# Kernel optimization log

Hardware: AMD Instinct MI355X
Metric: run time of the kernel (lower is better)

The kernel has to match this reference:

```python
import jax, jax.numpy as jnp
import numpy as np

B, L, DL, DM, K = 8192, 1, 1024, 1024, 8


def setup_inputs() -> dict:
    key = jax.random.key(0)
    ks = jax.random.split(key, 8)
    s = lambda k, shape, sc=1.0: jax.random.normal(k, shape, jnp.float32) * sc
    return {
        "l_hidden": s(ks[0], (B, L, DL)),
        "m_hidden": s(ks[1], (B, L, DM)),
        "G_l_m": s(ks[2], (DL, K, DM)),   # randn'd each fwd in torch; exposed as input
        "G_m_l": s(ks[3], (DM, K, DL)),
        "l_fc1_w": s(ks[4], (256, DL), 0.02),
        "l_fc1_b": jnp.zeros((256,), jnp.float32),
        "l_fc2_w": s(ks[5], (DL, 256), 0.02),
        "l_fc2_b": jnp.zeros((DL,), jnp.float32),
        "m_fc1_w": s(ks[6], (128, DM), 0.02),
        "m_fc1_b": jnp.zeros((128,), jnp.float32),
        "m_fc2_w": s(ks[7], (DM, 128), 0.02),
        "m_fc2_b": jnp.zeros((DM,), jnp.float32),
    }


def _cross(h_a, h_b, G, g_vec):
    """One direction of the cross-share unit.
    h_a: [B,L,Da], h_b: [B,L,Db], G: [Da,K,Db], g_vec: [B,L,Da]. L must be 1.
    Broadcasts G over batch instead of torch's .repeat (same math, no 256GB copy).
    """
    b, l, da = h_a.shape
    k = G.shape[1]
    # l_hidden @ reshape(G, [Da, K*Db]) -> reshape to [B, L*K, Db]
    s = jnp.einsum('bld,dke->blke', h_a, G).reshape(b, l * k, -1)      # [B,L*K,Db]
    # tanh( shared @ h_b^T ) -> [B, L*K, L]
    t = jnp.tanh(jnp.einsum('bke,bse->bks', s, h_b))                    # [B,L*K,L]
    # reshape [B,L,K,L] -> permute [B,L,L,K] -> [B,L*L,K]
    t = t.reshape(b, l, k, l).transpose(0, 1, 3, 2).reshape(b, l * l, k)
    g = jnp.tile(g_vec, (1, k, 1))                                      # [B,L*K,Da] (L=1 -> [B,K,Da])
    vec = jnp.matmul(t, g)                                              # [B,L*L,Da]
    attn = jax.nn.softmax(vec, axis=-1)
    out = h_a + attn * h_a
    return out, attn


def reference(l_hidden, m_hidden, G_l_m, G_m_l,
              l_fc1_w, l_fc1_b, l_fc2_w, l_fc2_b,
              m_fc1_w, m_fc1_b, m_fc2_w, m_fc2_b):
    # dropout(0.3) is identity in eval mode
    G_vec_l = (l_hidden @ l_fc1_w.T + l_fc1_b) @ l_fc2_w.T + l_fc2_b   # [B,L,DL]
    G_vec_m = (m_hidden @ m_fc1_w.T + m_fc1_b) @ m_fc2_w.T + m_fc2_b   # [B,L,DM]
    l_out, l_attn = _cross(l_hidden, m_hidden, G_l_m, G_vec_l)
    m_out, m_attn = _cross(m_hidden, l_hidden, G_m_l, G_vec_m)
    return l_out, m_out, l_attn, m_attn
```

## Files before the change

kernel.cpp:

```cpp
#include <hip/hip_runtime.h>


#define NB 8192
#define DD 1024

typedef __bf16 bf16x8 __attribute__((ext_vector_type(8)));
typedef float f32x4 __attribute__((ext_vector_type(4)));

__device__ __forceinline__ unsigned short f2bf(float f) {
  unsigned u = __float_as_uint(f);
  u += 0x7FFFu + ((u >> 16) & 1u);
  return (unsigned short)(u >> 16);
}
__device__ __forceinline__ float bf2f(unsigned short h) {
  return __uint_as_float(((unsigned)h) << 16);
}

__global__ __launch_bounds__(256) void split_cast_k(
    const float* __restrict__ in, unsigned short* __restrict__ hi,
    unsigned short* __restrict__ lo, int n4) {
  int i = blockIdx.x * 256 + threadIdx.x;
  if (i >= n4) return;
  float4 v = reinterpret_cast<const float4*>(in)[i];
  float vv[4] = {v.x, v.y, v.z, v.w};
  unsigned short hh[4], ll[4];
#pragma unroll
  for (int c = 0; c < 4; ++c) {
    hh[c] = f2bf(vv[c]);
    ll[c] = f2bf(vv[c] - bf2f(hh[c]));
  }
  reinterpret_cast<ushort4*>(hi)[i] = make_ushort4(hh[0], hh[1], hh[2], hh[3]);
  reinterpret_cast<ushort4*>(lo)[i] = make_ushort4(ll[0], ll[1], ll[2], ll[3]);
}

__global__ __launch_bounds__(256) void transpose_split_k(
    const float* __restrict__ G, unsigned short* __restrict__ bhi,
    unsigned short* __restrict__ blo) {
  __shared__ float t[32][33];
  int c0 = blockIdx.x * 32;
  int d0 = blockIdx.y * 32;
  int tx = threadIdx.x & 31;
  int tg = threadIdx.x >> 5;
#pragma unroll
  for (int s = 0; s < 4; ++s) {
    int dr = tg * 4 + s;
    t[dr][tx] = G[(size_t)(d0 + dr) * 8192 + c0 + tx];
  }
  __syncthreads();
#pragma unroll
  for (int s = 0; s < 4; ++s) {
    int cr = tg * 4 + s;
    float v = t[tx][cr];
    size_t o = (size_t)(c0 + cr) * 1024 + d0 + tx;
    unsigned short h = f2bf(v);
    bhi[o] = h;
    blo[o] = f2bf(v - bf2f(h));
  }
}

__global__ __launch_bounds__(256) void wct_k(
    const float* __restrict__ w1, const float* __restrict__ b1,
    const float* __restrict__ w2, const float* __restrict__ b2, int J,
    unsigned short* __restrict__ bhi, unsigned short* __restrict__ blo,
    float* __restrict__ bc) {
  __shared__ float w2row[256];
  int n = blockIdx.x;
  int tid = threadIdx.x;
  if (tid < J) w2row[tid] = w2[n * J + tid];
  __syncthreads();
#pragma unroll
  for (int s = 0; s < 4; ++s) {
    int i = tid + s * 256;
    float acc = 0.f;
    for (int j = 0; j < J; ++j) acc = fmaf(w2row[j], w1[j * 1024 + i], acc);
    size_t o = (size_t)(8192 + n) * 1024 + i;
    unsigned short h = f2bf(acc);
    bhi[o] = h;
    blo[o] = f2bf(acc - bf2f(h));
  }
  if (tid == 0) {
    float acc = 0.f;
    for (int j = 0; j < J; ++j) acc = fmaf(w2row[j], b1[j], acc);
    bc[n] = acc + b2[n];
  }
}

#define SBAR() do { asm volatile("" ::: "memory"); __builtin_amdgcn_s_barrier(); asm volatile("" ::: "memory"); } while (0)
#define WAITV4() asm volatile("s_waitcnt vmcnt(4)" ::: "memory")
#define WAITV6() asm volatile("s_waitcnt vmcnt(6)" ::: "memory")

#define GLOAD(SRC, DST)                                              \
  __builtin_amdgcn_global_load_lds(                                  \
      (const __attribute__((address_space(1))) void*)(SRC),          \
      (__attribute__((address_space(3))) void*)(lds + (DST)), 16, 0, 0)

__global__ __launch_bounds__(512, 2) void gemm_k(
    const unsigned short* __restrict__ Ahi_, const unsigned short* __restrict__ Alo_,
    const unsigned short* __restrict__ Bhi_, const unsigned short* __restrict__ Blo_,
    const float* __restrict__ hb, float* __restrict__ gvec, float* __restrict__ x) {
  __shared__ __align__(16) char lds[147456];
  const char* Ah = (const char*)Ahi_;
  const char* Al = (const char*)Alo_;
  const char* Bh = (const char*)Bhi_;
  const char* Bl = (const char*)Blo_;

  const int tid = threadIdx.x;
  const int lane = tid & 63;
  const int wid = tid >> 6;
  const int wm = wid >> 2, wn = wid & 3;

  const int bid = blockIdx.x;
  const int xcd = bid & 7, j = bid >> 3;
  const int by = xcd * 4 + (j & 3);
  const int bx = j >> 2;
  const int m0 = by * 256, n0 = bx * 256;
  const int nt = (n0 >= 8192) ? 16 : 48;

  const int rowl = tid >> 3;
  const int colsw = ((tid & 7) ^ ((tid >> 3) & 7)) << 4;
  const int s0 = ((lane >> 4) ^ (lane & 7)) << 4;
  const int s1 = s0 ^ 64;

  f32x4 acc[4][4][2] = {};

  auto stage = [&](int tile, int q) {
    if (tile < nt) {
      const int seg = tile >> 4;
      const char* mat;
      int rowbase, dst;
      if (q < 2) {
        mat = (seg == 1) ? Al : Ah;
        rowbase = m0 + q * 128;
        dst = (tile & 1) * 32768 + q * 16384;
      } else {
        mat = (seg == 2) ? Bl : Bh;
        rowbase = n0 + (q - 2) * 128;
        dst = 65536 + (tile & 1) * 32768 + (q - 2) * 16384;
      }
      const char* src = mat + (size_t)(rowbase + rowl) * 2048 + ((tile & 15) << 7) + colsw;
      dst += wid * 1024;
      GLOAD(src, dst);
      GLOAD(src + 64 * 2048, dst + 8192);
    } else {
      const char* src = Ah + (size_t)(m0 + rowl) * 2048 + colsw;
      const int d2 = 131072 + wid * 1024;
      GLOAD(src, d2);
      GLOAD(src + 64 * 2048, d2 + 8192);
    }
  };

  auto ldA = [&](bf16x8 (*d)[2], int qa, int cb) {
    const char* p = lds + cb + qa * 16384 + (wm * 64 + (lane & 15)) * 128;
#pragma unroll
    for (int f = 0; f < 4; ++f) {
      d[f][0] = *reinterpret_cast<const bf16x8*>(p + f * 2048 + s0);
      d[f][1] = *reinterpret_cast<const bf16x8*>(p + f * 2048 + s1);
    }
  };
  auto ldB = [&](bf16x8 (*d)[2], int qb, int cb) {
    const char* p = lds + 65536 + cb + qb * 16384 + (wn * 32 + (lane & 15)) * 128;
#pragma unroll
    for (int g = 0; g < 2; ++g) {
      d[g][0] = *reinterpret_cast<const bf16x8*>(p + g * 2048 + s0);
      d[g][1] = *reinterpret_cast<const bf16x8*>(p + g * 2048 + s1);
    }
  };
  auto mm = [&](f32x4 (*ac)[2], bf16x8 (*aa)[2], bf16x8 (*bb)[2]) {
#pragma unroll
    for (int f = 0; f < 4; ++f)
#pragma unroll
      for (int g = 0; g < 2; ++g) {
        ac[f][g] = __builtin_amdgcn_mfma_f32_16x16x32_bf16(aa[f][0], bb[g][0], ac[f][g], 0, 0, 0);
        ac[f][g] = __builtin_amdgcn_mfma_f32_16x16x32_bf16(aa[f][1], bb[g][1], ac[f][g], 0, 0, 0);
      }
  };

  stage(0, 0); stage(0, 2);
  stage(0, 3);
  stage(0, 1);
  WAITV4();
  SBAR();

  bf16x8 af[4][2], af2[4][2], bv[2][2], bv2[2][2];
  for (int t = 0; t < nt; ++t) {
    const int cb = (t & 1) * 32768;
    ldA(af, 0, cb);
    ldB(bv, 0, cb);
    stage(t + 1, 0); stage(t + 1, 2);
    SBAR();
    __builtin_amdgcn_s_setprio(1);
    mm(acc[0], af, bv);
    __builtin_amdgcn_s_setprio(0);
    WAITV6();
    SBAR();
    ldB(bv2, 1, cb);
    stage(t + 1, 3);
    SBAR();
    __builtin_amdgcn_s_setprio(1);
    mm(acc[1], af, bv2);
    __builtin_amdgcn_s_setprio(0);
    WAITV6();
    SBAR();
    ldA(af2, 1, cb);
    stage(t + 1, 1);
    SBAR();
    __builtin_amdgcn_s_setprio(1);
    mm(acc[2], af2, bv2);
    __builtin_amdgcn_s_setprio(0);
    SBAR();
    ldB(bv, 0, cb);
    SBAR();
    __builtin_amdgcn_s_setprio(1);
    mm(acc[3], af2, bv);
    __builtin_amdgcn_s_setprio(0);
    WAITV4();
    SBAR();
  }

  const int coll = lane & 15;
  const int rg = (lane >> 4) * 4;
  if (n0 >= 8192) {
#pragma unroll
    for (int q = 0; q < 4; ++q) {
      const int qm = (q >= 2);
      const int qn = (q == 1 || q == 2);
#pragma unroll
      for (int f = 0; f < 4; ++f)
#pragma unroll
        for (int r = 0; r < 4; ++r) {
          const int row = m0 + qm * 128 + wm * 64 + f * 16 + rg + r;
#pragma unroll
          for (int g = 0; g < 2; ++g) {
            const int gcol = (n0 - 8192) + qn * 128 + wn * 32 + g * 16 + coll;
            gvec[(size_t)row * 1024 + gcol] = acc[q][f][g][r];
          }
        }
    }
  } else {
    const int kidx = n0 >> 10;
    const int ebase = (n0 & 1023) + wn * 32 + coll;
#pragma unroll
    for (int qm = 0; qm < 2; ++qm) {
      f32x4 (*acA)[2] = acc[qm ? 3 : 0];
      f32x4 (*acB)[2] = acc[qm ? 2 : 1];
#pragma unroll
      for (int f = 0; f < 4; ++f)
#pragma unroll
        for (int r = 0; r < 4; ++r) {
          const int row = m0 + qm * 128 + wm * 64 + f * 16 + rg + r;
          const float* hr = hb + (size_t)row * 1024 + ebase;
          float tmp = acA[f][0][r] * hr[0] + acA[f][1][r] * hr[16] +
                      acB[f][0][r] * hr[128] + acB[f][1][r] * hr[144];
#pragma unroll
          for (int s = 1; s < 16; s <<= 1) tmp += __shfl_xor(tmp, s);
          if (coll == 0) atomicAdd(&x[row * 8 + kidx], tmp);
        }
    }
  }
}

__global__ __launch_bounds__(256) void finalize_k(
    const float* __restrict__ xk, const float* __restrict__ gvec,
    const float* __restrict__ bc, const float* __restrict__ ha,
    float* __restrict__ out, float* __restrict__ attn) {
  int b = blockIdx.x;
  int tid = threadIdx.x;
  float S = 0.f;
#pragma unroll
  for (int k = 0; k < 8; ++k) S += tanhf(xk[b * 8 + k]);
  float v[4];
  float mx = -3.4e38f;
#pragma unroll
  for (int s = 0; s < 4; ++s) {
    int d = tid + s * 256;
    v[s] = S * (gvec[(size_t)b * 1024 + d] + bc[d]);
    mx = fmaxf(mx, v[s]);
  }
  __shared__ float red[8];
#pragma unroll
  for (int off = 32; off >= 1; off >>= 1) mx = fmaxf(mx, __shfl_xor(mx, off));
  int lane = tid & 63, w = tid >> 6;
  if (lane == 0) red[w] = mx;
  __syncthreads();
  float m = fmaxf(fmaxf(red[0], red[1]), fmaxf(red[2], red[3]));
  float e[4], sum = 0.f;
#pragma unroll
  for (int s = 0; s < 4; ++s) { e[s] = __expf(v[s] - m); sum += e[s]; }
#pragma unroll
  for (int off = 32; off >= 1; off >>= 1) sum += __shfl_xor(sum, off);
  if (lane == 0) red[4 + w] = sum;
  __syncthreads();
  float inv = 1.f / (red[4] + red[5] + red[6] + red[7]);
#pragma unroll
  for (int s = 0; s < 4; ++s) {
    int d = tid + s * 256;
    float a = e[s] * inv;
    attn[(size_t)b * 1024 + d] = a;
    float h = ha[(size_t)b * 1024 + d];
    out[(size_t)b * 1024 + d] = fmaf(a, h, h);
  }
}

extern "C" void kernel_launch(void* const* d_in, const int* in_sizes, int n_in,
                              void* d_out, int out_size, void* d_ws, size_t ws_size,
                              hipStream_t stream) {
  const float* l_hidden = (const float*)d_in[0];
  const float* m_hidden = (const float*)d_in[1];
  const float* G_l_m = (const float*)d_in[2];
  const float* G_m_l = (const float*)d_in[3];
  const float* l_fc1_w = (const float*)d_in[4];
  const float* l_fc1_b = (const float*)d_in[5];
  const float* l_fc2_w = (const float*)d_in[6];
  const float* l_fc2_b = (const float*)d_in[7];
  const float* m_fc1_w = (const float*)d_in[8];
  const float* m_fc1_b = (const float*)d_in[9];
  const float* m_fc2_w = (const float*)d_in[10];
  const float* m_fc2_b = (const float*)d_in[11];
  float* out = (float*)d_out;

  char* ws = (char*)d_ws;
  unsigned short* Ahi = (unsigned short*)(ws);
  unsigned short* Alo = (unsigned short*)(ws + 16777216);
  unsigned short* Bhi = (unsigned short*)(ws + 33554432);
  unsigned short* Blo = (unsigned short*)(ws + 52428800);
  float* gvec = (float*)(ws + 71303168);
  float* x = (float*)(ws + 104857600);
  float* bc = (float*)(ws + 105381888);

  hipMemsetAsync(x, 0, 2 * NB * 8 * sizeof(float), stream);

  const size_t BD = (size_t)NB * DD;
  dim3 gemmGrid(1152);

  split_cast_k<<<(int)(BD / 4 / 256), 256, 0, stream>>>(l_hidden, Ahi, Alo, (int)(BD / 4));
  transpose_split_k<<<dim3(256, 32), 256, 0, stream>>>(G_l_m, Bhi, Blo);
  wct_k<<<1024, 256, 0, stream>>>(l_fc1_w, l_fc1_b, l_fc2_w, l_fc2_b, 256, Bhi, Blo, bc);
  gemm_k<<<gemmGrid, 512, 0, stream>>>(Ahi, Alo, Bhi, Blo, m_hidden, gvec, x);
  finalize_k<<<NB, 256, 0, stream>>>(x, gvec, bc, l_hidden, out, out + 2 * BD);

  split_cast_k<<<(int)(BD / 4 / 256), 256, 0, stream>>>(m_hidden, Ahi, Alo, (int)(BD / 4));
  transpose_split_k<<<dim3(256, 32), 256, 0, stream>>>(G_m_l, Bhi, Blo);
  wct_k<<<1024, 256, 0, stream>>>(m_fc1_w, m_fc1_b, m_fc2_w, m_fc2_b, 128, Bhi, Blo, bc);
  gemm_k<<<gemmGrid, 512, 0, stream>>>(Ahi, Alo, Bhi, Blo, l_hidden, gvec, x + NB * 8);
  finalize_k<<<NB, 256, 0, stream>>>(x + NB * 8, gvec, bc, m_hidden, out + BD, out + 3 * BD);
}
```

Baseline: 1.095 ms.

## Split three-pass bf16x3 GEMM K-loop across separate blocks with simpler pipeline

Each of the three hi/lo precision passes (hi*hi, lo*hi, hi*lo) for the G-projection tiles now runs in its own block, with results combined through the existing atomicAdd into x. This triples the block count for that part and shortens each block's K loop from 48 to 16 tiles. The software pipeline is also simplified: all four quarter-tile loads for the next stage are issued up front, with a single vmcnt(0) wait and one barrier per iteration instead of the fine-grained interleaved waits and barriers. This removes the extra LDS buffer that held the A tile for the epilogue, cutting shared memory from 147456 to 131072 bytes. The trade-off is more atomics and more redundant epilogue reads of hb, plus a coarser load/compute overlap that may expose memory latency.

```diff
diff --git a/kernel.cpp b/kernel.cpp
--- a/kernel.cpp
+++ b/kernel.cpp
@@ -86,8 +86,7 @@
 }
 
 #define SBAR() do { asm volatile("" ::: "memory"); __builtin_amdgcn_s_barrier(); asm volatile("" ::: "memory"); } while (0)
-#define WAITV4() asm volatile("s_waitcnt vmcnt(4)" ::: "memory")
-#define WAITV6() asm volatile("s_waitcnt vmcnt(6)" ::: "memory")
+#define WAITV0() asm volatile("s_waitcnt vmcnt(0)" ::: "memory")
 
 #define GLOAD(SRC, DST)                                              \
   __builtin_amdgcn_global_load_lds(                                  \
@@ -98,7 +97,7 @@
     const unsigned short* __restrict__ Ahi_, const unsigned short* __restrict__ Alo_,
     const unsigned short* __restrict__ Bhi_, const unsigned short* __restrict__ Blo_,
     const float* __restrict__ hb, float* __restrict__ gvec, float* __restrict__ x) {
-  __shared__ __align__(16) char lds[147456];
+  __shared__ __align__(16) char lds[131072];
   const char* Ah = (const char*)Ahi_;
   const char* Al = (const char*)Alo_;
   const char* Bh = (const char*)Bhi_;
@@ -110,11 +109,18 @@
   const int wm = wid >> 2, wn = wid & 3;
 
   const int bid = blockIdx.x;
-  const int xcd = bid & 7, j = bid >> 3;
-  const int by = xcd * 4 + (j & 3);
-  const int bx = j >> 2;
-  const int m0 = by * 256, n0 = bx * 256;
-  const int nt = (n0 >= 8192) ? 16 : 48;
+  const int xcd = bid & 7;
+  const int j = bid >> 3;
+  const bool isg = (j >= 384);
+  const int r = isg ? (j - 384) : (j & 127);
+  const int seg = isg ? 0 : (j >> 7);
+  const int by = xcd * 4 + (r & 3);
+  const int bx = r >> 2;
+  const int m0 = by * 256;
+  const int n0 = isg ? (8192 + bx * 256) : (bx * 256);
+
+  const char* Ab = (seg == 1) ? Al : Ah;
+  const char* Bb = (seg == 2) ? Bl : Bh;
 
   const int rowl = tid >> 3;
   const int colsw = ((tid & 7) ^ ((tid >> 3) & 7)) << 4;
@@ -123,30 +129,22 @@
 
   f32x4 acc[4][4][2] = {};
 
-  auto stage = [&](int tile, int q) {
-    if (tile < nt) {
-      const int seg = tile >> 4;
-      const char* mat;
-      int rowbase, dst;
-      if (q < 2) {
-        mat = (seg == 1) ? Al : Ah;
-        rowbase = m0 + q * 128;
-        dst = (tile & 1) * 32768 + q * 16384;
-      } else {
-        mat = (seg == 2) ? Bl : Bh;
-        rowbase = n0 + (q - 2) * 128;
-        dst = 65536 + (tile & 1) * 32768 + (q - 2) * 16384;
-      }
-      const char* src = mat + (size_t)(rowbase + rowl) * 2048 + ((tile & 15) << 7) + colsw;
-      dst += wid * 1024;
-      GLOAD(src, dst);
-      GLOAD(src + 64 * 2048, dst + 8192);
+  auto stage = [&](int tl, int q) {
+    const char* mat;
+    int rowbase, dst;
+    if (q < 2) {
+      mat = Ab;
+      rowbase = m0 + q * 128;
+      dst = (tl & 1) * 32768 + q * 16384;
     } else {
-      const char* src = Ah + (size_t)(m0 + rowl) * 2048 + colsw;
-      const int d2 = 131072 + wid * 1024;
-      GLOAD(src, d2);
-      GLOAD(src + 64 * 2048, d2 + 8192);
-    }
+      mat = Bb;
+      rowbase = n0 + (q - 2) * 128;
+      dst = 65536 + (tl & 1) * 32768 + (q - 2) * 16384;
+    }
+    const char* src = mat + (size_t)(rowbase + rowl) * 2048 + (tl << 7) + colsw;
+    dst += wid * 1024;
+    GLOAD(src, dst);
+    GLOAD(src + 64 * 2048, dst + 8192);
   };
 
   auto ldA = [&](bf16x8 (*d)[2], int qa, int cb) {
@@ -175,51 +173,35 @@
       }
   };
 
-  stage(0, 0); stage(0, 2);
-  stage(0, 3);
-  stage(0, 1);
-  WAITV4();
+  stage(0, 0); stage(0, 1); stage(0, 2); stage(0, 3);
+  WAITV0();
   SBAR();
 
   bf16x8 af[4][2], af2[4][2], bv[2][2], bv2[2][2];
-  for (int t = 0; t < nt; ++t) {
+  for (int t = 0; t < 16; ++t) {
     const int cb = (t & 1) * 32768;
+    if (t < 15) {
+      stage(t + 1, 0); stage(t + 1, 1); stage(t + 1, 2); stage(t + 1, 3);
+    }
     ldA(af, 0, cb);
     ldB(bv, 0, cb);
-    stage(t + 1, 0); stage(t + 1, 2);
-    SBAR();
+    ldB(bv2, 1, cb);
     __builtin_amdgcn_s_setprio(1);
     mm(acc[0], af, bv);
     __builtin_amdgcn_s_setprio(0);
-    WAITV6();
-    SBAR();
-    ldB(bv2, 1, cb);
-    stage(t + 1, 3);
-    SBAR();
+    ldA(af2, 1, cb);
     __builtin_amdgcn_s_setprio(1);
     mm(acc[1], af, bv2);
-    __builtin_amdgcn_s_setprio(0);
-    WAITV6();
-    SBAR();
-    ldA(af2, 1, cb);
-    stage(t + 1, 1);
-    SBAR();
-    __builtin_amdgcn_s_setprio(1);
     mm(acc[2], af2, bv2);
-    __builtin_amdgcn_s_setprio(0);
-    SBAR();
-    ldB(bv, 0, cb);
-    SBAR();
-    __builtin_amdgcn_s_setprio(1);
     mm(acc[3], af2, bv);
     __builtin_amdgcn_s_setprio(0);
-    WAITV4();
+    WAITV0();
     SBAR();
   }
 
   const int coll = lane & 15;
   const int rg = (lane >> 4) * 4;
-  if (n0 >= 8192) {
+  if (isg) {
 #pragma unroll
     for (int q = 0; q < 4; ++q) {
       const int qm = (q >= 2);
@@ -227,12 +209,12 @@
 #pragma unroll
       for (int f = 0; f < 4; ++f)
 #pragma unroll
-        for (int r = 0; r < 4; ++r) {
-          const int row = m0 + qm * 128 + wm * 64 + f * 16 + rg + r;
+        for (int rr = 0; rr < 4; ++rr) {
+          const int row = m0 + qm * 128 + wm * 64 + f * 16 + rg + rr;
 #pragma unroll
           for (int g = 0; g < 2; ++g) {
             const int gcol = (n0 - 8192) + qn * 128 + wn * 32 + g * 16 + coll;
-            gvec[(size_t)row * 1024 + gcol] = acc[q][f][g][r];
+            gvec[(size_t)row * 1024 + gcol] = acc[q][f][g][rr];
           }
         }
     }
@@ -246,11 +228,11 @@
 #pragma unroll
       for (int f = 0; f < 4; ++f)
 #pragma unroll
-        for (int r = 0; r < 4; ++r) {
-          const int row = m0 + qm * 128 + wm * 64 + f * 16 + rg + r;
+        for (int rr = 0; rr < 4; ++rr) {
+          const int row = m0 + qm * 128 + wm * 64 + f * 16 + rg + rr;
           const float* hr = hb + (size_t)row * 1024 + ebase;
-          float tmp = acA[f][0][r] * hr[0] + acA[f][1][r] * hr[16] +
-                      acB[f][0][r] * hr[128] + acB[f][1][r] * hr[144];
+          float tmp = acA[f][0][rr] * hr[0] + acA[f][1][rr] * hr[16] +
+                      acB[f][0][rr] * hr[128] + acB[f][1][rr] * hr[144];
 #pragma unroll
           for (int s = 1; s < 16; s <<= 1) tmp += __shfl_xor(tmp, s);
           if (coll == 0) atomicAdd(&x[row * 8 + kidx], tmp);
@@ -330,7 +312,7 @@
   hipMemsetAsync(x, 0, 2 * NB * 8 * sizeof(float), stream);
 
   const size_t BD = (size_t)NB * DD;
-  dim3 gemmGrid(1152);
+  dim3 gemmGrid(3200);
 
   split_cast_k<<<(int)(BD / 4 / 256), 256, 0, stream>>>(l_hidden, Ahi, Alo, (int)(BD / 4));
   transpose_split_k<<<dim3(256, 32), 256, 0, stream>>>(G_l_m, Bhi, Blo);
```

Result: slower. 1.357 ms (+23.9%).
